# Optimization experiments

Hardware: AMD Instinct MI355X
Metric: run time of the kernel (lower is better)

Reference implementation:

```python
import jax, jax.numpy as jnp
import numpy as np

N = 50000      # n_nodes
E = 800000     # n_edges
D = 64         # in_dim == out_dim
K = 3          # k-neighbourhoods {1,2,3} at t=2
T = 2          # layer index t
NU = 1         # cfg.nu -> delay(k) = max(k - nu, 0)
AGG_EPS = 1e-6
BN_EPS = 1e-5


def setup_inputs() -> dict:
    key = jax.random.key(0)
    ks = jax.random.split(key, 8)
    xs = jax.random.normal(ks[0], (T + 1, N, D), dtype=jnp.float32)
    edge_index = jax.random.randint(ks[1], (2, E), 0, N, dtype=jnp.int32)
    edge_attr = jax.random.randint(ks[2], (E,), 1, K + 1, dtype=jnp.int32)  # hop k in {1..K}
    s = 1.0 / np.sqrt(D)
    Wa = jax.random.normal(ks[3], (D, D), dtype=jnp.float32) * s
    Wd = jax.random.normal(ks[4], (D, D), dtype=jnp.float32) * s
    Wb = jax.random.normal(ks[5], (K, D, D), dtype=jnp.float32) * s
    return {
        "xs": xs,
        "edge_index": edge_index,
        "edge_attr": edge_attr,
        "Wa": Wa, "ba": jnp.zeros((D,), jnp.float32),
        "Wd": Wd, "bd": jnp.zeros((D,), jnp.float32),
        "Wb": Wb, "bb": jnp.zeros((K, D), jnp.float32),
        "gamma": jnp.ones((D,), jnp.float32),
        "beta": jnp.zeros((D,), jnp.float32),
    }


def reference(xs, edge_index, edge_attr, Wa, ba, Wd, bd, Wb, bb, gamma, beta):
    # current node state
    x = xs[T]  # [N, D]
    # delayed state per hop k: xs[t - max(k - nu, 0)] -> indices [2, 1, 0] for k = 1,2,3
    state_idx = jnp.array([T - max(k - NU, 0) for k in range(1, K + 1)])
    states = xs[state_idx]                                   # [K, N, D]
    # per-k linear B_k (source uses B for both Bx and Ex)
    Bx = jnp.einsum('knd,kdo->kno', states, Wb) + bb[:, None, :]  # [K, N, D]
    Ex = Bx
    Ax = x @ Wa + ba                                         # [N, D]
    Dx = x @ Wd + bd                                         # [N, D]

    i_idx = edge_index[1]                                    # destination
    j_idx = edge_index[0]                                    # source
    ke = edge_attr - 1                                       # [E], 0..K-1

    Dx_i = Dx[i_idx]                                         # [E, D]
    Ex_j = Ex[ke, j_idx]                                     # [E, D] per-k gather
    Bx_j = Bx[ke, j_idx]                                     # [E, D]

    sigma = jax.nn.sigmoid(Dx_i + Ex_j)                      # [E, D]

    # per-(node, k) scatter-sum; segment id packs (i, k)
    seg = i_idx * K + ke
    num = jax.ops.segment_sum(sigma * Bx_j, seg, num_segments=N * K).reshape(N, K, D)
    den = jax.ops.segment_sum(sigma, seg, num_segments=N * K).reshape(N, K, D)
    eta = num / (den + AGG_EPS)                              # [N, K, D]

    alpha = 1.0 / K  # softmax(ones(K)) with convex combination
    x_new = Ax + alpha * eta.sum(axis=1)                     # [N, D]

    # BatchNorm1d over nodes (training-mode batch statistics, biased var)
    mean = x_new.mean(axis=0)
    var = jnp.var(x_new, axis=0)
    y = gamma * (x_new - mean) * jax.lax.rsqrt(var + BN_EPS) + beta
    return jax.nn.relu(y)  # dropout p=0.0, residual=False
```

## Files before the change

kernel.cpp:

```cpp
#include <hip/hip_runtime.h>
#include <hip/hip_bf16.h>

#define D 64
#define K 3

typedef __hip_bfloat16 bf16;

__device__ __forceinline__ float b2f(bf16 v) { return __bfloat162float(v); }

__device__ __forceinline__ unsigned short f2bf(float f)
{
    const unsigned x = __float_as_uint(f);
    return (unsigned short)((x + 0x7FFFu + ((x >> 16) & 1u)) >> 16);
}

#define P_WA 0
#define P_BA 4096
#define P_WD 4160
#define P_BD 8256
#define P_WB 8320
#define P_BB 20608
#define P_G  20800
#define P_B  20864
#define P_TOTAL 20928

#define LOG2E 1.442695041f

#define NB_MAX 1024
#define BKN    128
#define BKSEG  (BKN * K)

__global__ void cvt_hist_kernel(const void* Wa, const void* ba, const void* Wd, const void* bd,
                                const void* Wb, const void* bb, const void* g, const void* b,
                                float* __restrict__ P, int* __restrict__ flag,
                                const int* __restrict__ ei,
                                int* __restrict__ bcnt, int* __restrict__ bbase,
                                int* __restrict__ bcur, int* __restrict__ off,
                                int* __restrict__ done,
                                int E, int M, int HB, int cb, int NB)
{
    __shared__ int bins[NB_MAX];
    __shared__ int lastret;
    const int bid = blockIdx.x;
    const int tid = threadIdx.x;

    if (bid < HB) {
        for (int i = tid; i < NB; i += 256) bins[i] = 0;
        __syncthreads();
        const int tstr = HB * 256;
        for (int e = bid * 256 + tid; e < E; e += tstr)
            atomicAdd(&bins[ei[E + e] >> 7], 1);
        __syncthreads();
        for (int i = tid; i < NB; i += 256) {
            const int c = bins[i];
            if (c) atomicAdd(&bcnt[i], c);
        }
        __threadfence();
        __syncthreads();
        if (tid == 0) lastret = atomicAdd(done, 1);
        __syncthreads();
        if (lastret == HB - 1) {
            __threadfence();
            const int base = tid * 4;
            int v[4];
            #pragma unroll
            for (int q = 0; q < 4; q++) {
                const int i = base + q;
                v[q] = (i < NB) ? bcnt[i] : 0;
            }
            const int tsum = v[0] + v[1] + v[2] + v[3];
            bins[tid] = tsum;
            __syncthreads();
            #pragma unroll
            for (int o = 1; o < 256; o <<= 1) {
                int x = (tid >= o) ? bins[tid - o] : 0;
                __syncthreads();
                bins[tid] += x;
                __syncthreads();
            }
            int run = bins[tid] - tsum;
            #pragma unroll
            for (int q = 0; q < 4; q++) {
                const int i = base + q;
                if (i < NB) { bbase[i] = run; bcur[i] = run; }
                run += v[q];
            }
            if (tid == 0) off[M] = E;
        }
        return;
    }

    const int isbf = (((const unsigned int*)g)[0] == 0x3F803F80u) ? 1 : 0;
    if (bid == HB && tid == 0) *flag = isbf;
    int i = (bid - HB) * 256 + tid;
    const int stride = cb * 256;
    for (; i < P_TOTAL; i += stride) {
        const void* src; int off_;
        if (i < P_BA)      { src = Wa; off_ = i; }
        else if (i < P_WD) { src = ba; off_ = i - P_BA; }
        else if (i < P_BD) { src = Wd; off_ = i - P_WD; }
        else if (i < P_WB) { src = bd; off_ = i - P_BD; }
        else if (i < P_BB) { src = Wb; off_ = i - P_WB; }
        else if (i < P_G)  { src = bb; off_ = i - P_BB; }
        else if (i < P_B)  { src = g;  off_ = i - P_G; }
        else               { src = b;  off_ = i - P_B; }
        float v;
        if (isbf) v = b2f(((const bf16*)src)[off_]);
        else      v = ((const float*)src)[off_];
        P[i] = v;
    }
}

union U8 { float4 f; ushort4 u; };

__device__ __forceinline__ void lin_load(U8 reg[8], const void* xs_raw, size_t xbase,
                                         int isbf, int tid, int nbase, int N)
{
    if (isbf) {
        const ushort* xp = (const ushort*)xs_raw + xbase;
        #pragma unroll
        for (int p = 0; p < 8; p++) {
            const int idx = tid + (p << 8);
            const int n = nbase + (idx >> 4), c4 = (idx & 15) << 2;
            if (n < N) reg[p].u = *(const ushort4*)(xp + (size_t)n * D + c4);
            else       reg[p].u = make_ushort4(0, 0, 0, 0);
        }
    } else {
        const float* xp = (const float*)xs_raw + xbase;
        #pragma unroll
        for (int p = 0; p < 8; p++) {
            const int idx = tid + (p << 8);
            const int n = nbase + (idx >> 4), c4 = (idx & 15) << 2;
            if (n < N) reg[p].f = *(const float4*)(xp + (size_t)n * D + c4);
            else       reg[p].f = make_float4(0.f, 0.f, 0.f, 0.f);
        }
    }
}

__global__ void lin_binscat_kernel(const void* __restrict__ xs_raw,
                                   const float* __restrict__ P, const int* __restrict__ flag,
                                   float* __restrict__ Ax, float* __restrict__ Dx,
                                   void* __restrict__ Bx, int N,
                                   const int* __restrict__ ei, const int* __restrict__ ea,
                                   int* __restrict__ bcur, int* __restrict__ bkt,
                                   int E, int NB, int CH, int SB, int gx)
{
    __shared__ __align__(16) char smem[49920];
    const int bid = blockIdx.x;
    const int tid = threadIdx.x;

    if (bid < SB) {
        int* lcnt  = (int*)smem;
        int* lbase = (int*)(smem + 4096);
        const int s0 = bid * CH;
        int s1 = s0 + CH; if (s1 > E) s1 = E;

        for (int i = tid; i < NB; i += 256) lcnt[i] = 0;
        __syncthreads();
        for (int e = s0 + tid; e < s1; e += 256)
            atomicAdd(&lcnt[ei[E + e] >> 7], 1);
        __syncthreads();
        for (int b = tid; b < NB; b += 256) {
            const int c = lcnt[b];
            lbase[b] = c ? atomicAdd(&bcur[b], c) : 0;
            lcnt[b] = 0;
        }
        __syncthreads();
        for (int e = s0 + tid; e < s1; e += 256) {
            const int i  = ei[E + e];
            const int j  = ei[e];
            const int ke = ea[e] - 1;
            const int b  = i >> 7;
            const int r  = atomicAdd(&lcnt[b], 1);
            bkt[lbase[b] + r] = ((i & 127) << 19) | (ke << 17) | j;
        }
        return;
    }

    float (*sw)[64] = (float(*)[64])smem;
    float (*sx)[65] = (float(*)[65])(smem + 16384);
    float* sbias    = (float*)(smem + 49664);

    const int isbf = *flag;
    const int lb = bid - SB;
    const int which = lb / gx;
    const int t0    = lb % gx;
    const size_t ND = (size_t)N * D;

    const float* W; const float* bias; size_t xbase;
    float* outf = nullptr; ushort* outh = nullptr;
    if (which == 0)      { W = P + P_WA; bias = P + P_BA; xbase = 2 * ND; outf = Ax; }
    else if (which == 1) { W = P + P_WD; bias = P + P_BD; xbase = 2 * ND; outf = Dx; }
    else {
        const int k = which - 2;
        W = P + P_WB + (size_t)k * D * D;
        bias = P + P_BB + (size_t)k * D;
        const int layer = 2 - k;
        xbase = (size_t)layer * ND;
        if (isbf) outh = (ushort*)Bx + k * ND;
        else      outf = (float*)Bx + k * ND;
    }
    const int bfout = (outh != nullptr);

    for (int idx = tid; idx < D * D; idx += 256)
        sw[idx >> 6][idx & 63] = W[idx];
    if (tid < 64) sbias[tid] = bias[tid];

    const int tiles = (N + 127) >> 7;

    U8 reg[8];
    int t = t0;
    if (t < tiles) lin_load(reg, xs_raw, xbase, isbf, tid, t << 7, N);

    const int ct = tid & 7;  const int c0 = ct * 8;
    const int nt = tid >> 3; const int n0 = nt * 4;

    for (; t < tiles; t += gx) {
        __syncthreads();
        #pragma unroll
        for (int p = 0; p < 8; p++) {
            const int idx = tid + (p << 8);
            const int n = idx >> 4, c4 = (idx & 15) << 2;
            float v0, v1, v2, v3;
            if (isbf) {
                v0 = __uint_as_float((unsigned)reg[p].u.x << 16);
                v1 = __uint_as_float((unsigned)reg[p].u.y << 16);
                v2 = __uint_as_float((unsigned)reg[p].u.z << 16);
                v3 = __uint_as_float((unsigned)reg[p].u.w << 16);
            } else {
                v0 = reg[p].f.x; v1 = reg[p].f.y; v2 = reg[p].f.z; v3 = reg[p].f.w;
            }
            sx[n][c4 + 0] = v0; sx[n][c4 + 1] = v1;
            sx[n][c4 + 2] = v2; sx[n][c4 + 3] = v3;
        }
        __syncthreads();

        const int tn = t + gx;
        if (tn < tiles) lin_load(reg, xs_raw, xbase, isbf, tid, tn << 7, N);

        float acc[4][8];
        {
            float b0[8];
            #pragma unroll
            for (int j = 0; j < 8; j++) b0[j] = sbias[c0 + j];
            #pragma unroll
            for (int i = 0; i < 4; i++)
                #pragma unroll
                for (int j = 0; j < 8; j++) acc[i][j] = b0[j];
        }

        #pragma unroll 8
        for (int kk = 0; kk < 64; kk++) {
            const float4 wlo = *(const float4*)&sw[kk][c0];
            const float4 whi = *(const float4*)&sw[kk][c0 + 4];
            float xv[4];
            #pragma unroll
            for (int i = 0; i < 4; i++) xv[i] = sx[n0 + i][kk];
            #pragma unroll
            for (int i = 0; i < 4; i++) {
                acc[i][0] += xv[i] * wlo.x; acc[i][1] += xv[i] * wlo.y;
                acc[i][2] += xv[i] * wlo.z; acc[i][3] += xv[i] * wlo.w;
                acc[i][4] += xv[i] * whi.x; acc[i][5] += xv[i] * whi.y;
                acc[i][6] += xv[i] * whi.z; acc[i][7] += xv[i] * whi.w;
            }
        }

        const int nbase = t << 7;
        #pragma unroll
        for (int i = 0; i < 4; i++) {
            const int gn = nbase + n0 + i;
            if (gn < N) {
                if (bfout) {
                    ushort* op = outh + (size_t)gn * D + c0;
                    *(ushort4*)op = make_ushort4(f2bf(acc[i][0]), f2bf(acc[i][1]),
                                                 f2bf(acc[i][2]), f2bf(acc[i][3]));
                    *(ushort4*)(op + 4) = make_ushort4(f2bf(acc[i][4]), f2bf(acc[i][5]),
                                                       f2bf(acc[i][6]), f2bf(acc[i][7]));
                } else {
                    float* op = outf + (size_t)gn * D + c0;
                    *(float4*)op       = make_float4(acc[i][0], acc[i][1], acc[i][2], acc[i][3]);
                    *(float4*)(op + 4) = make_float4(acc[i][4], acc[i][5], acc[i][6], acc[i][7]);
                }
            }
        }
    }
}

__global__ void bucketsort_kernel(const int* __restrict__ bbase, const int* __restrict__ bcur,
                                  const int* __restrict__ bkt,
                                  int* __restrict__ off, int* __restrict__ elist, int M)
{
    __shared__ int cl[512];
    __shared__ int cu[512];
    const int b = blockIdx.x, tid = threadIdx.x;
    const int s0 = bbase[b], s1 = bcur[b];

    cl[tid] = 0; cl[tid + 256] = 0;
    __syncthreads();
    for (int idx = s0 + tid; idx < s1; idx += 256) {
        const int p = bkt[idx];
        atomicAdd(&cl[(p >> 19) * 3 + ((p >> 17) & 3)], 1);
    }
    __syncthreads();
    const int c0 = cl[tid], c1 = cl[tid + 256];
    for (int o = 1; o < 512; o <<= 1) {
        const int a0 = (tid >= o) ? cl[tid - o] : 0;
        const int a1 = cl[tid + 256 - o];
        __syncthreads();
        cl[tid] += a0; cl[tid + 256] += a1;
        __syncthreads();
    }
    const int e0 = cl[tid] - c0, e1 = cl[tid + 256] - c1;
    cu[tid] = e0; cu[tid + 256] = e1;
    const int gbase = b * BKSEG;
    {
        const int gs0 = gbase + tid;
        if (tid < BKSEG && gs0 < M) off[gs0] = s0 + e0;
        const int ls1 = tid + 256;
        const int gs1 = gbase + ls1;
        if (ls1 < BKSEG && gs1 < M) off[gs1] = s0 + e1;
    }
    __syncthreads();
    for (int idx = s0 + tid; idx < s1; idx += 256) {
        const int p = bkt[idx];
        const int ls = (p >> 19) * 3 + ((p >> 17) & 3);
        const int pos = atomicAdd(&cu[ls], 1);
        elist[s0 + pos] = p & 0x1FFFF;
    }
}

template<int BF>
__device__ __forceinline__ float ldbx(const void* bxk, int j, int d)
{
    if (BF) {
        const ushort u = ((const ushort*)bxk)[((size_t)(unsigned)j << 6) + d];
        return __uint_as_float((unsigned)u << 16);
    }
    return ((const float*)bxk)[((size_t)(unsigned)j << 6) + d];
}

template<int BF>
__device__ __forceinline__ float node_eta(const void* __restrict__ Bx, size_t ND,
                                          const int* __restrict__ elist,
                                          int o0, int o1, int o2, int o3,
                                          int d, float ndx)
{
    int wb = o0;
    int jv = (wb + d < o3) ? elist[wb + d] : 0;
    float eta = 0.f;
    #pragma unroll
    for (int k = 0; k < K; k++) {
        const void* bxk = (const char*)Bx + (size_t)k * ND * (BF ? 2 : 4);
        const int sbeg = (k == 0) ? o0 : (k == 1) ? o1 : o2;
        const int send = (k == 0) ? o1 : (k == 1) ? o2 : o3;
        float num = 0.f, den = 0.f;
        int p = sbeg;
        while (p < send) {
            if (p - wb >= 64) {
                wb = p;
                jv = (wb + d < o3) ? elist[wb + d] : 0;
            }
            int lim = wb + 64; if (lim > send) lim = send;
            int c = p - wb;
            const int cend = lim - wb;
            for (; c + 3 < cend; c += 4) {
                const int j0 = __builtin_amdgcn_readlane(jv, c);
                const int j1 = __builtin_amdgcn_readlane(jv, c + 1);
                const int j2 = __builtin_amdgcn_readlane(jv, c + 2);
                const int j3 = __builtin_amdgcn_readlane(jv, c + 3);
                const float bx0 = ldbx<BF>(bxk, j0, d);
                const float bx1 = ldbx<BF>(bxk, j1, d);
                const float bx2 = ldbx<BF>(bxk, j2, d);
                const float bx3 = ldbx<BF>(bxk, j3, d);
                const float s0 = __builtin_amdgcn_rcpf(1.f + __builtin_amdgcn_exp2f(fmaf(bx0, -LOG2E, ndx)));
                const float s1 = __builtin_amdgcn_rcpf(1.f + __builtin_amdgcn_exp2f(fmaf(bx1, -LOG2E, ndx)));
                const float s2 = __builtin_amdgcn_rcpf(1.f + __builtin_amdgcn_exp2f(fmaf(bx2, -LOG2E, ndx)));
                const float s3 = __builtin_amdgcn_rcpf(1.f + __builtin_amdgcn_exp2f(fmaf(bx3, -LOG2E, ndx)));
                num = fmaf(s0, bx0, num); den += s0;
                num = fmaf(s1, bx1, num); den += s1;
                num = fmaf(s2, bx2, num); den += s2;
                num = fmaf(s3, bx3, num); den += s3;
            }
            for (; c < cend; ++c) {
                const int j0 = __builtin_amdgcn_readlane(jv, c);
                const float bx0 = ldbx<BF>(bxk, j0, d);
                const float s0 = __builtin_amdgcn_rcpf(1.f + __builtin_amdgcn_exp2f(fmaf(bx0, -LOG2E, ndx)));
                num = fmaf(s0, bx0, num); den += s0;
            }
            p = lim;
        }
        eta = fmaf(num, __builtin_amdgcn_rcpf(den + 1e-6f), eta);
    }
    return eta;
}

__global__ void node_kernel(float* __restrict__ Ax,
                            const float* __restrict__ Dx, const void* __restrict__ Bx,
                            const int* __restrict__ off, const int* __restrict__ elist,
                            float* __restrict__ statsP, const int* __restrict__ flag, int N)
{
    __shared__ float red[256];
    const int tid = threadIdx.x;
    const int w = tid >> 6, d = tid & 63;
    const size_t ND = (size_t)N * D;
    const int isbf = *flag;

    float lsum = 0.f, lsq = 0.f;
    for (int n = blockIdx.x * 4 + w; n < N; n += gridDim.x * 4) {
        const float dx = Dx[(size_t)n * D + d];
        const float ndx = dx * -LOG2E;
        const int b0 = n * 3;
        const int o0 = off[b0];
        const int o1 = off[b0 + 1];
        const int o2 = off[b0 + 2];
        const int o3 = off[b0 + 3];
        const float eta = isbf ? node_eta<1>(Bx, ND, elist, o0, o1, o2, o3, d, ndx)
                               : node_eta<0>(Bx, ND, elist, o0, o1, o2, o3, d, ndx);
        const size_t xi = (size_t)n * D + d;
        const float v = Ax[xi] + eta * (1.f / 3.f);
        Ax[xi] = v;
        lsum += v;
        lsq  += v * v;
    }

    red[tid] = lsum;
    __syncthreads();
    if (tid < 64) {
        float* sp = statsP + (size_t)(blockIdx.x & 63) * 128;
        atomicAdd(&sp[d], red[d] + red[64 + d] + red[128 + d] + red[192 + d]);
    }
    __syncthreads();
    red[tid] = lsq;
    __syncthreads();
    if (tid < 64) {
        float* sp = statsP + (size_t)(blockIdx.x & 63) * 128;
        atomicAdd(&sp[64 + d], red[d] + red[64 + d] + red[128 + d] + red[192 + d]);
    }
}

__global__ void finalize_kernel(const float* __restrict__ xnew, const float* __restrict__ statsP,
                                const float* __restrict__ P, const int* __restrict__ flag,
                                void* __restrict__ out, int N)
{
    __shared__ float sstats[128];
    const int tid = threadIdx.x;
    if (tid < 128) {
        float a = 0.f;
        for (int c = 0; c < 64; c++) a += statsP[c * 128 + tid];
        sstats[tid] = a;
    }
    __syncthreads();

    const float invN = 1.f / (float)N;
    const int isbf = *flag;
    const long long total = (long long)N * D;
    for (long long gidx = (long long)blockIdx.x * 256 + tid; gidx < total;
         gidx += (long long)gridDim.x * 256) {
        const int d = (int)(gidx & 63);
        const float mean = sstats[d] * invN;
        const float var  = sstats[64 + d] * invN - mean * mean;
        const float rstd = rsqrtf(var + 1e-5f);
        float y = P[P_G + d] * (xnew[gidx] - mean) * rstd + P[P_B + d];
        y = fmaxf(y, 0.f);
        if (isbf) ((bf16*)out)[gidx] = __float2bfloat16(y);
        else      ((float*)out)[gidx] = y;
    }
}

extern "C" void kernel_launch(void* const* d_in, const int* in_sizes, int n_in,
                              void* d_out, int out_size, void* d_ws, size_t ws_size,
                              hipStream_t stream)
{
    const void* xs = d_in[0];
    const int*  ei = (const int*)d_in[1];
    const int*  ea = (const int*)d_in[2];

    const int N = in_sizes[0] / (3 * D);
    const int E = in_sizes[2];
    const int M = N * K;
    const int NB = (N + BKN - 1) / BKN;

    float* ws = (float*)d_ws;
    const size_t nd = (size_t)N * D;

    float* P      = ws;
    int*   flag   = (int*)(P + P_TOTAL);
    float* Ax     = (float*)(flag + 1);
    float* Dx     = Ax + nd;
    float* Bx     = Dx + nd;
    float* statsP = Bx + 3 * nd;
    int*   bcnt   = (int*)(statsP + 64 * 128);
    int*   done   = bcnt + NB_MAX;
    int*   bbase  = done + 2;
    int*   bcur   = bbase + NB_MAX;
    int*   off    = bcur + NB_MAX;
    int*   bkt    = off + (M + 1);
    int*   elist  = bkt + E;

    const size_t zbytes = (size_t)(64 * 128 + NB_MAX + 2) * 4;
    hipMemsetAsync(statsP, 0, zbytes, stream);

    const int HB = 256;
    const int cb = 82;
    cvt_hist_kernel<<<HB + cb, 256, 0, stream>>>(
        d_in[3], d_in[4], d_in[5], d_in[6], d_in[7], d_in[8], d_in[9], d_in[10],
        P, flag, ei, bcnt, bbase, bcur, off, done, E, M, HB, cb, NB);

    const int tiles = (N + 127) / 128;
    const int gx = (tiles < 144) ? tiles : 144;
    const int LB = gx * 5;
    const int SB = 128;
    const int CH = (E + SB - 1) / SB;
    lin_binscat_kernel<<<SB + LB, 256, 0, stream>>>(xs, P, flag, Ax, Dx, (void*)Bx, N,
                                                    ei, ea, bcur, bkt, E, NB, CH, SB, gx);

    bucketsort_kernel<<<NB, 256, 0, stream>>>(bbase, bcur, bkt, off, elist, M);

    node_kernel<<<2048, 256, 0, stream>>>(Ax, Dx, (const void*)Bx, off, elist,
                                          statsP, flag, N);

    finalize_kernel<<<2048, 256, 0, stream>>>(Ax, statsP, P, flag, d_out, N);
}
```

Before: 241.4 us.

## Use bf16 MFMA for node linear transforms instead of LDS-tiled FP32 FMA

Replaces the shared-memory tiled scalar FP32 GEMM for the Ax/Dx/Bx projections with MFMA 16x16x32 bf16 instructions. Weights are kept in registers as bf16 fragments, and each wave loads its input rows directly from global memory, so the LDS staging and barriers go away. The tile size changes to 64 rows, and the fp32-input path becomes a naive per-thread loop. Weights are rounded to bf16, which lowers precision. Output stores are scalar with a stride, so they are less coalesced.

Result: slower. 460.0 us (+90.5%).

```diff
diff --git a/kernel.cpp b/kernel.cpp
--- a/kernel.cpp
+++ b/kernel.cpp
@@ -5,6 +5,8 @@
 #define K 3
 
 typedef __hip_bfloat16 bf16;
+typedef __attribute__((ext_vector_type(8))) short bf16x8;
+typedef __attribute__((ext_vector_type(4))) float f32x4;
 
 __device__ __forceinline__ float b2f(bf16 v) { return __bfloat162float(v); }
 
@@ -111,32 +113,6 @@
     }
 }
 
-union U8 { float4 f; ushort4 u; };
-
-__device__ __forceinline__ void lin_load(U8 reg[8], const void* xs_raw, size_t xbase,
-                                         int isbf, int tid, int nbase, int N)
-{
-    if (isbf) {
-        const ushort* xp = (const ushort*)xs_raw + xbase;
-        #pragma unroll
-        for (int p = 0; p < 8; p++) {
-            const int idx = tid + (p << 8);
-            const int n = nbase + (idx >> 4), c4 = (idx & 15) << 2;
-            if (n < N) reg[p].u = *(const ushort4*)(xp + (size_t)n * D + c4);
-            else       reg[p].u = make_ushort4(0, 0, 0, 0);
-        }
-    } else {
-        const float* xp = (const float*)xs_raw + xbase;
-        #pragma unroll
-        for (int p = 0; p < 8; p++) {
-            const int idx = tid + (p << 8);
-            const int n = nbase + (idx >> 4), c4 = (idx & 15) << 2;
-            if (n < N) reg[p].f = *(const float4*)(xp + (size_t)n * D + c4);
-            else       reg[p].f = make_float4(0.f, 0.f, 0.f, 0.f);
-        }
-    }
-}
-
 __global__ void lin_binscat_kernel(const void* __restrict__ xs_raw,
                                    const float* __restrict__ P, const int* __restrict__ flag,
                                    float* __restrict__ Ax, float* __restrict__ Dx,
@@ -145,13 +121,12 @@
                                    int* __restrict__ bcur, int* __restrict__ bkt,
                                    int E, int NB, int CH, int SB, int gx)
 {
-    __shared__ __align__(16) char smem[49920];
+    __shared__ int lcnt[NB_MAX];
+    __shared__ int lbase[NB_MAX];
     const int bid = blockIdx.x;
     const int tid = threadIdx.x;
 
     if (bid < SB) {
-        int* lcnt  = (int*)smem;
-        int* lbase = (int*)(smem + 4096);
         const int s0 = bid * CH;
         int s1 = s0 + CH; if (s1 > E) s1 = E;
 
@@ -176,10 +151,6 @@
         }
         return;
     }
-
-    float (*sw)[64] = (float(*)[64])smem;
-    float (*sx)[65] = (float(*)[65])(smem + 16384);
-    float* sbias    = (float*)(smem + 49664);
 
     const int isbf = *flag;
     const int lb = bid - SB;
@@ -201,86 +172,73 @@
         else      outf = (float*)Bx + k * ND;
     }
     const int bfout = (outh != nullptr);
-
-    for (int idx = tid; idx < D * D; idx += 256)
-        sw[idx >> 6][idx & 63] = W[idx];
-    if (tid < 64) sbias[tid] = bias[tid];
-
-    const int tiles = (N + 127) >> 7;
-
-    U8 reg[8];
-    int t = t0;
-    if (t < tiles) lin_load(reg, xs_raw, xbase, isbf, tid, t << 7, N);
-
-    const int ct = tid & 7;  const int c0 = ct * 8;
-    const int nt = tid >> 3; const int n0 = nt * 4;
-
-    for (; t < tiles; t += gx) {
-        __syncthreads();
+    const int tiles = (N + 63) >> 6;
+
+    if (isbf) {
+        const ushort* xp = (const ushort*)xs_raw + xbase;
+        const int wid  = tid >> 6;
+        const int lane = tid & 63;
+        const int lm = lane & 15;
+        const int lk = lane >> 4;
+
+        bf16x8 bf[2][4];
         #pragma unroll
-        for (int p = 0; p < 8; p++) {
-            const int idx = tid + (p << 8);
-            const int n = idx >> 4, c4 = (idx & 15) << 2;
-            float v0, v1, v2, v3;
-            if (isbf) {
-                v0 = __uint_as_float((unsigned)reg[p].u.x << 16);
-                v1 = __uint_as_float((unsigned)reg[p].u.y << 16);
-                v2 = __uint_as_float((unsigned)reg[p].u.z << 16);
-                v3 = __uint_as_float((unsigned)reg[p].u.w << 16);
-            } else {
-                v0 = reg[p].f.x; v1 = reg[p].f.y; v2 = reg[p].f.z; v3 = reg[p].f.w;
-            }
-            sx[n][c4 + 0] = v0; sx[n][c4 + 1] = v1;
-            sx[n][c4 + 2] = v2; sx[n][c4 + 3] = v3;
-        }
-        __syncthreads();
-
-        const int tn = t + gx;
-        if (tn < tiles) lin_load(reg, xs_raw, xbase, isbf, tid, tn << 7, N);
-
-        float acc[4][8];
-        {
-            float b0[8];
-            #pragma unroll
-            for (int j = 0; j < 8; j++) b0[j] = sbias[c0 + j];
-            #pragma unroll
-            for (int i = 0; i < 4; i++)
+        for (int kt = 0; kt < 2; kt++)
+            #pragma unroll
+            for (int ct = 0; ct < 4; ct++)
                 #pragma unroll
-                for (int j = 0; j < 8; j++) acc[i][j] = b0[j];
-        }
-
-        #pragma unroll 8
-        for (int kk = 0; kk < 64; kk++) {
-            const float4 wlo = *(const float4*)&sw[kk][c0];
-            const float4 whi = *(const float4*)&sw[kk][c0 + 4];
-            float xv[4];
-            #pragma unroll
-            for (int i = 0; i < 4; i++) xv[i] = sx[n0 + i][kk];
-            #pragma unroll
-            for (int i = 0; i < 4; i++) {
-                acc[i][0] += xv[i] * wlo.x; acc[i][1] += xv[i] * wlo.y;
-                acc[i][2] += xv[i] * wlo.z; acc[i][3] += xv[i] * wlo.w;
-                acc[i][4] += xv[i] * whi.x; acc[i][5] += xv[i] * whi.y;
-                acc[i][6] += xv[i] * whi.z; acc[i][7] += xv[i] * whi.w;
-            }
-        }
-
-        const int nbase = t << 7;
+                for (int j = 0; j < 8; j++)
+                    bf[kt][ct][j] = (short)f2bf(W[(kt * 32 + lk * 8 + j) * 64 + ct * 16 + lm]);
+
+        float bias_v[4];
         #pragma unroll
-        for (int i = 0; i < 4; i++) {
-            const int gn = nbase + n0 + i;
-            if (gn < N) {
-                if (bfout) {
-                    ushort* op = outh + (size_t)gn * D + c0;
-                    *(ushort4*)op = make_ushort4(f2bf(acc[i][0]), f2bf(acc[i][1]),
-                                                 f2bf(acc[i][2]), f2bf(acc[i][3]));
-                    *(ushort4*)(op + 4) = make_ushort4(f2bf(acc[i][4]), f2bf(acc[i][5]),
-                                                       f2bf(acc[i][6]), f2bf(acc[i][7]));
-                } else {
-                    float* op = outf + (size_t)gn * D + c0;
-                    *(float4*)op       = make_float4(acc[i][0], acc[i][1], acc[i][2], acc[i][3]);
-                    *(float4*)(op + 4) = make_float4(acc[i][4], acc[i][5], acc[i][6], acc[i][7]);
+        for (int ct = 0; ct < 4; ct++) bias_v[ct] = bias[ct * 16 + lm];
+
+        for (int t = t0; t < tiles; t += gx) {
+            const int n0 = t * 64 + wid * 16;
+            int row = n0 + lm; if (row >= N) row = N - 1;
+            const ushort* ap = xp + (size_t)row * 64 + lk * 8;
+            const bf16x8 a0 = *(const bf16x8*)ap;
+            const bf16x8 a1 = *(const bf16x8*)(ap + 32);
+
+            f32x4 acc[4];
+            #pragma unroll
+            for (int ct = 0; ct < 4; ct++) {
+                acc[ct][0] = bias_v[ct]; acc[ct][1] = bias_v[ct];
+                acc[ct][2] = bias_v[ct]; acc[ct][3] = bias_v[ct];
+            }
+            #pragma unroll
+            for (int ct = 0; ct < 4; ct++)
+                acc[ct] = __builtin_amdgcn_mfma_f32_16x16x32_bf16(a0, bf[0][ct], acc[ct], 0, 0, 0);
+            #pragma unroll
+            for (int ct = 0; ct < 4; ct++)
+                acc[ct] = __builtin_amdgcn_mfma_f32_16x16x32_bf16(a1, bf[1][ct], acc[ct], 0, 0, 0);
+
+            #pragma unroll
+            for (int ct = 0; ct < 4; ct++) {
+                const int c = ct * 16 + lm;
+                #pragma unroll
+                for (int i = 0; i < 4; i++) {
+                    const int r = n0 + lk * 4 + i;
+                    if (r < N) {
+                        if (bfout) outh[(size_t)r * 64 + c] = f2bf(acc[ct][i]);
+                        else       outf[(size_t)r * 64 + c] = acc[ct][i];
+                    }
                 }
+            }
+        }
+    } else {
+        const float* xp = (const float*)xs_raw + xbase;
+        const int c = tid & 63;
+        for (int t = t0; t < tiles; t += gx) {
+            const int n0 = t * 64;
+            for (int rr = tid >> 6; rr < 64; rr += 4) {
+                const int r = n0 + rr;
+                if (r >= N) break;
+                float acc = bias[c];
+                for (int kk = 0; kk < 64; kk++)
+                    acc = fmaf(xp[(size_t)r * 64 + kk], W[kk * 64 + c], acc);
+                outf[(size_t)r * 64 + c] = acc;
             }
         }
     }
@@ -506,7 +464,7 @@
         d_in[3], d_in[4], d_in[5], d_in[6], d_in[7], d_in[8], d_in[9], d_in[10],
         P, flag, ei, bcnt, bbase, bcur, off, done, E, M, HB, cb, NB);
 
-    const int tiles = (N + 127) / 128;
+    const int tiles = (N + 63) / 64;
     const int gx = (tiles < 144) ? tiles : 144;
     const int LB = gx * 5;
     const int SB = 128;
```

## Store bf16 tiles and weights in LDS and widen linear-layer grid

Applied to the files above, without the earlier changes.

On the bf16 path, the linear-transform blocks now keep both the input tile and the weight matrix in LDS as raw bf16 and convert to float at use. This halves shared memory per block from about 49KB to 25KB, so more blocks can be resident per CU. The grid width per transform doubles so more blocks cover the tiles. The fp32 path becomes a simple unshared per-thread loop. The bf16 path also rounds the weights to bf16, which loses precision.

After: 492.4 us. +104.0%, slower.

```diff
diff --git a/kernel.cpp b/kernel.cpp
--- a/kernel.cpp
+++ b/kernel.cpp
@@ -5,6 +5,7 @@
 #define K 3
 
 typedef __hip_bfloat16 bf16;
+typedef __attribute__((ext_vector_type(8))) unsigned short u16x8;
 
 __device__ __forceinline__ float b2f(bf16 v) { return __bfloat162float(v); }
 
@@ -12,6 +13,11 @@
 {
     const unsigned x = __float_as_uint(f);
     return (unsigned short)((x + 0x7FFFu + ((x >> 16) & 1u)) >> 16);
+}
+
+__device__ __forceinline__ float bfu(unsigned short u)
+{
+    return __uint_as_float((unsigned)u << 16);
 }
 
 #define P_WA 0
@@ -111,32 +117,6 @@
     }
 }
 
-union U8 { float4 f; ushort4 u; };
-
-__device__ __forceinline__ void lin_load(U8 reg[8], const void* xs_raw, size_t xbase,
-                                         int isbf, int tid, int nbase, int N)
-{
-    if (isbf) {
-        const ushort* xp = (const ushort*)xs_raw + xbase;
-        #pragma unroll
-        for (int p = 0; p < 8; p++) {
-            const int idx = tid + (p << 8);
-            const int n = nbase + (idx >> 4), c4 = (idx & 15) << 2;
-            if (n < N) reg[p].u = *(const ushort4*)(xp + (size_t)n * D + c4);
-            else       reg[p].u = make_ushort4(0, 0, 0, 0);
-        }
-    } else {
-        const float* xp = (const float*)xs_raw + xbase;
-        #pragma unroll
-        for (int p = 0; p < 8; p++) {
-            const int idx = tid + (p << 8);
-            const int n = nbase + (idx >> 4), c4 = (idx & 15) << 2;
-            if (n < N) reg[p].f = *(const float4*)(xp + (size_t)n * D + c4);
-            else       reg[p].f = make_float4(0.f, 0.f, 0.f, 0.f);
-        }
-    }
-}
-
 __global__ void lin_binscat_kernel(const void* __restrict__ xs_raw,
                                    const float* __restrict__ P, const int* __restrict__ flag,
                                    float* __restrict__ Ax, float* __restrict__ Dx,
@@ -145,7 +125,7 @@
                                    int* __restrict__ bcur, int* __restrict__ bkt,
                                    int E, int NB, int CH, int SB, int gx)
 {
-    __shared__ __align__(16) char smem[49920];
+    __shared__ __align__(16) char smem[25856];
     const int bid = blockIdx.x;
     const int tid = threadIdx.x;
 
@@ -177,9 +157,9 @@
         return;
     }
 
-    float (*sw)[64] = (float(*)[64])smem;
-    float (*sx)[65] = (float(*)[65])(smem + 16384);
-    float* sbias    = (float*)(smem + 49664);
+    ushort* sw_u      = (ushort*)smem;
+    ushort (*sx_u)[68] = (ushort(*)[68])(smem + 8192);
+    float* sbias      = (float*)(smem + 8192 + 17408);
 
     const int isbf = *flag;
     const int lb = bid - SB;
@@ -201,16 +181,42 @@
         else      outf = (float*)Bx + k * ND;
     }
     const int bfout = (outh != nullptr);
-
-    for (int idx = tid; idx < D * D; idx += 256)
-        sw[idx >> 6][idx & 63] = W[idx];
+    const int tiles = (N + 127) >> 7;
+
+    if (!isbf) {
+        const float* xp = (const float*)xs_raw + xbase;
+        const int c = tid & 63;
+        for (int t = t0; t < tiles; t += gx) {
+            const int n0 = t * 128;
+            for (int rr = tid >> 6; rr < 128; rr += 4) {
+                const int r = n0 + rr;
+                if (r >= N) break;
+                float acc = bias[c];
+                for (int kk = 0; kk < 64; kk++)
+                    acc = fmaf(xp[(size_t)r * 64 + kk], W[kk * 64 + c], acc);
+                outf[(size_t)r * 64 + c] = acc;
+            }
+        }
+        return;
+    }
+
+    const ushort* xp = (const ushort*)xs_raw + xbase;
+    for (int idx = tid; idx < 4096; idx += 256)
+        sw_u[idx] = f2bf(W[idx]);
     if (tid < 64) sbias[tid] = bias[tid];
 
-    const int tiles = (N + 127) >> 7;
-
-    U8 reg[8];
+    ushort4 reg[8];
     int t = t0;
-    if (t < tiles) lin_load(reg, xs_raw, xbase, isbf, tid, t << 7, N);
+    if (t < tiles) {
+        const int nbase = t << 7;
+        #pragma unroll
+        for (int p = 0; p < 8; p++) {
+            const int idx = tid + (p << 8);
+            const int n = nbase + (idx >> 4), c4 = (idx & 15) << 2;
+            reg[p] = (n < N) ? *(const ushort4*)(xp + (size_t)n * D + c4)
+                             : make_ushort4(0, 0, 0, 0);
+        }
+    }
 
     const int ct = tid & 7;  const int c0 = ct * 8;
     const int nt = tid >> 3; const int n0 = nt * 4;
@@ -221,22 +227,21 @@
         for (int p = 0; p < 8; p++) {
             const int idx = tid + (p << 8);
             const int n = idx >> 4, c4 = (idx & 15) << 2;
-            float v0, v1, v2, v3;
-            if (isbf) {
-                v0 = __uint_as_float((unsigned)reg[p].u.x << 16);
-                v1 = __uint_as_float((unsigned)reg[p].u.y << 16);
-                v2 = __uint_as_float((unsigned)reg[p].u.z << 16);
-                v3 = __uint_as_float((unsigned)reg[p].u.w << 16);
-            } else {
-                v0 = reg[p].f.x; v1 = reg[p].f.y; v2 = reg[p].f.z; v3 = reg[p].f.w;
-            }
-            sx[n][c4 + 0] = v0; sx[n][c4 + 1] = v1;
-            sx[n][c4 + 2] = v2; sx[n][c4 + 3] = v3;
+            *(ushort4*)&sx_u[n][c4] = reg[p];
         }
         __syncthreads();
 
         const int tn = t + gx;
-        if (tn < tiles) lin_load(reg, xs_raw, xbase, isbf, tid, tn << 7, N);
+        if (tn < tiles) {
+            const int nbase = tn << 7;
+            #pragma unroll
+            for (int p = 0; p < 8; p++) {
+                const int idx = tid + (p << 8);
+                const int n = nbase + (idx >> 4), c4 = (idx & 15) << 2;
+                reg[p] = (n < N) ? *(const ushort4*)(xp + (size_t)n * D + c4)
+                                 : make_ushort4(0, 0, 0, 0);
+            }
+        }
 
         float acc[4][8];
         {
@@ -251,17 +256,19 @@
 
         #pragma unroll 8
         for (int kk = 0; kk < 64; kk++) {
-            const float4 wlo = *(const float4*)&sw[kk][c0];
-            const float4 whi = *(const float4*)&sw[kk][c0 + 4];
+            const u16x8 wv = *(const u16x8*)&sw_u[kk * 64 + c0];
+            float w[8];
+            #pragma unroll
+            for (int j = 0; j < 8; j++) w[j] = bfu(wv[j]);
             float xv[4];
             #pragma unroll
-            for (int i = 0; i < 4; i++) xv[i] = sx[n0 + i][kk];
+            for (int i = 0; i < 4; i++) xv[i] = bfu(sx_u[n0 + i][kk]);
             #pragma unroll
             for (int i = 0; i < 4; i++) {
-                acc[i][0] += xv[i] * wlo.x; acc[i][1] += xv[i] * wlo.y;
-                acc[i][2] += xv[i] * wlo.z; acc[i][3] += xv[i] * wlo.w;
-                acc[i][4] += xv[i] * whi.x; acc[i][5] += xv[i] * whi.y;
-                acc[i][6] += xv[i] * whi.z; acc[i][7] += xv[i] * whi.w;
+                acc[i][0] += xv[i] * w[0]; acc[i][1] += xv[i] * w[1];
+                acc[i][2] += xv[i] * w[2]; acc[i][3] += xv[i] * w[3];
+                acc[i][4] += xv[i] * w[4]; acc[i][5] += xv[i] * w[5];
+                acc[i][6] += xv[i] * w[6]; acc[i][7] += xv[i] * w[7];
             }
         }
 
@@ -507,7 +514,7 @@
         P, flag, ei, bcnt, bbase, bcur, off, done, E, M, HB, cb, NB);
 
     const int tiles = (N + 127) / 128;
-    const int gx = (tiles < 144) ? tiles : 144;
+    const int gx = (tiles < 282) ? tiles : 282;
     const int LB = gx * 5;
     const int SB = 128;
     const int CH = (E + SB - 1) / SB;
```
